# Optimization experiments

Measured on AMD Instinct MI355X. Metric: run time of the kernel, lower is better.

The kernel has to match this reference:

```python
import jax, jax.numpy as jnp
import numpy as np

N = 50000   # nodes
E = 800000  # edges (avg degree 16)
H = 128     # hidden


def setup_inputs() -> dict:
    key = jax.random.key(0)
    k1, k2, k3, k4, k5 = jax.random.split(key, 5)
    s = 1.0 / np.sqrt(H).astype(np.float32)
    x = jax.random.normal(k1, (N, H), dtype=jnp.float32)
    edge_index = jax.random.randint(k2, (2, E), 0, N, dtype=jnp.int64)
    a_i = jax.random.normal(k3, (H,), dtype=jnp.float32) * s
    a_j = jax.random.normal(k4, (H,), dtype=jnp.float32) * s
    W = jax.random.normal(k5, (H, H), dtype=jnp.float32) * s
    return {"x": x, "edge_index": edge_index, "a_i": a_i, "a_j": a_j, "W": W}


def reference(x, edge_index, a_i, a_j, W):
    n = x.shape[0]
    idx_j = edge_index[0]  # row of sparse adj (output node)
    idx_i = edge_index[1]  # col of sparse adj (source node, softmax segment)

    # per-node attention scores, gathered per edge
    si = x @ a_i  # [N]
    sj = x @ a_j  # [N]
    e = jax.nn.leaky_relu(si[idx_i] + sj[idx_j], negative_slope=0.01)  # [E]

    # segment softmax over idx_i (numerically stable)
    seg_max = jax.ops.segment_max(e, idx_i, num_segments=n)
    e_exp = jnp.exp(e - seg_max[idx_i])
    denom = jax.ops.segment_sum(e_exp, idx_i, num_segments=n)
    alpha = e_exp / denom[idx_i]  # [E]

    # messages and sparse aggregation: out[j] += alpha * m[i]
    m = x + x @ W  # [N, H]
    out = jax.ops.segment_sum(alpha[:, None] * m[idx_i], idx_j, num_segments=n)

    # exact (erf) GELU to match torch nn.GELU default; dropout is identity in eval
    return jax.nn.gelu(out, approximate=False)
```

## Files before the change

kernel.cpp:

```cpp
#include <hip/hip_runtime.h>
#include <hip/hip_fp16.h>
#include <math.h>

#define HDIM 128
#define NB   32
#define CAP  768
#define BINB 256
#define DG   64
#define WIN  12544

typedef __attribute__((ext_vector_type(8))) short short8;
typedef __attribute__((ext_vector_type(4))) float f32x4;

__device__ __forceinline__ float gelu_f(float v) {
    return 0.5f * v * (1.0f + erff(v * 0.70710678118654752440f));
}
__device__ __forceinline__ unsigned bf_rne(float f) {
    unsigned u = __float_as_uint(f);
    return (u + 0x7fffu + ((u >> 16) & 1u)) >> 16;
}
__device__ __forceinline__ float bf_lo(unsigned u) {
    return __uint_as_float(u << 16);
}
__device__ __forceinline__ float bf_hi(unsigned u) {
    return __uint_as_float(u & 0xffff0000u);
}

__global__ void __launch_bounds__(256) k_scores(
    const float* __restrict__ x, const float* __restrict__ a_i,
    const float* __restrict__ a_j, float* __restrict__ si,
    float* __restrict__ sj, unsigned* __restrict__ xbp,
    unsigned* __restrict__ gcnt, int N) {
    if (blockIdx.x == 0)
        for (int w = threadIdx.x; w < 2048; w += 256) gcnt[w] = 0u;
    const int wave = threadIdx.x >> 6;
    const int lane = threadIdx.x & 63;
    const int n = blockIdx.x * 4 + wave;
    if (n >= N) return;
    const float xa = x[(size_t)n * HDIM + lane];
    const float xb = x[(size_t)n * HDIM + 64 + lane];
    xbp[(size_t)n * 64 + lane] = bf_rne(xa) | (bf_rne(xb) << 16);
    float vi = xa * a_i[lane] + xb * a_i[64 + lane];
    float vj = xa * a_j[lane] + xb * a_j[64 + lane];
    #pragma unroll
    for (int d = 32; d; d >>= 1) {
        vi += __shfl_xor(vi, d, 64);
        vj += __shfl_xor(vj, d, 64);
    }
    if (lane == 0) {
        si[n] = vi;
        sj[n] = vj;
    }
}

__global__ void __launch_bounds__(1024) k_bin(
    const int* __restrict__ idx_i, const int* __restrict__ idx_j,
    const float* __restrict__ si, const float* __restrict__ sj,
    unsigned short* __restrict__ exbuf, unsigned* __restrict__ gcnt,
    uint2* __restrict__ edges, int nbuk, int E_) {
    __shared__ unsigned cnt_l[2048];
    const int blk = blockIdx.x;
    const int chunk = (E_ + BINB - 1) / BINB;
    const int e0 = blk * chunk;
    const int e1 = min(e0 + chunk, E_);
    for (int w = threadIdx.x; w < nbuk; w += 1024) cnt_l[w] = 0u;
    __syncthreads();
    uint2 rec[4];
    int   bl[4];
    #pragma unroll
    for (int k = 0; k < 4; ++k) {
        const int t = e0 + threadIdx.x + k * 1024;
        bl[k] = -1;
        if (t < e1) {
            const int i = idx_i[t];
            const int j = idx_j[t];
            float e = si[i] + sj[j];
            e = (e > 0.f) ? e : 0.01f * e;
            const float ex = __expf(e);
            exbuf[t] = __half_as_ushort(__float2half(ex));
            const int b = j >> 5;
            atomicAdd(&cnt_l[b], 1u);
            rec[k] = make_uint2((unsigned)i | ((unsigned)(j & 31) << 24),
                                __float_as_uint(ex));
            bl[k] = b;
        }
    }
    for (int t = e0 + threadIdx.x + 4 * 1024; t < e1; t += 1024) {
        const int i = idx_i[t];
        const int j = idx_j[t];
        float e = si[i] + sj[j];
        e = (e > 0.f) ? e : 0.01f * e;
        const float ex = __expf(e);
        exbuf[t] = __half_as_ushort(__float2half(ex));
        const int b = j >> 5;
        const unsigned slot = min(atomicAdd(&gcnt[b], 1u), (unsigned)(CAP - 1));
        edges[(size_t)b * CAP + slot] = make_uint2(
            (unsigned)i | ((unsigned)(j & 31) << 24), __float_as_uint(ex));
    }
    __syncthreads();
    for (int w = threadIdx.x; w < nbuk; w += 1024) {
        const unsigned c = cnt_l[w];
        cnt_l[w] = c ? atomicAdd(&gcnt[w], c) : 0u;
    }
    __syncthreads();
    #pragma unroll
    for (int k = 0; k < 4; ++k) {
        if (bl[k] >= 0) {
            const unsigned slot =
                min(atomicAdd(&cnt_l[bl[k]], 1u), (unsigned)(CAP - 1));
            edges[(size_t)bl[k] * CAP + slot] = rec[k];
        }
    }
}

__global__ void __launch_bounds__(1024) k_den(
    const int* __restrict__ idx_i, const unsigned short* __restrict__ exbuf,
    float* __restrict__ denp, int N, int E_) {
    __shared__ float dl[WIN];
    const int b = blockIdx.x;
    const int chunk = (E_ + DG - 1) / DG;
    const int e0 = b * chunk;
    const int e1 = min(e0 + chunk, E_);
    for (int pass = 0; pass < 4; ++pass) {
        const int lo = pass * WIN;
        for (int w = threadIdx.x; w < WIN; w += 1024) dl[w] = 0.f;
        __syncthreads();
        for (int t = e0 + threadIdx.x; t < e1; t += 1024) {
            const int i = idx_i[t];
            const unsigned rel = (unsigned)(i - lo);
            if (rel < (unsigned)WIN)
                atomicAdd(&dl[rel], __half2float(__ushort_as_half(exbuf[t])));
        }
        __syncthreads();
        for (int w = threadIdx.x; w < WIN && lo + w < N; w += 1024)
            denp[(size_t)b * N + lo + w] = dl[w];
        __syncthreads();
    }
}

__global__ void __launch_bounds__(256) k_denred(const float* __restrict__ denp,
                                                float* __restrict__ denom,
                                                int N) {
    const int v = blockIdx.x * 256 + threadIdx.x;
    if (v >= N) return;
    float s = 0.f;
    for (int b = 0; b < DG; ++b) s += denp[(size_t)b * N + v];
    denom[v] = s;
}

__global__ void __launch_bounds__(256) k_gemm(
    const unsigned* __restrict__ xbp, const float* __restrict__ Wm,
    const float* __restrict__ denom, unsigned* __restrict__ mbp, int N) {
    __shared__ unsigned wl[128][68];
    const int t = threadIdx.x;
    {
        const int n = t & 127;
        const int h = t >> 7;
        for (int w = h * 32; w < h * 32 + 32; ++w) {
            const float f0 = Wm[w * 128 + n];
            const float f1 = Wm[(w + 64) * 128 + n];
            wl[n][w] = bf_rne(f0) | (bf_rne(f1) << 16);
        }
    }
    __syncthreads();
    const int wave = t >> 6;
    const int lane = t & 63;
    const int q = lane >> 4;
    const int m16 = lane & 15;
    const int r0 = blockIdx.x * 64 + wave * 16;
    if (r0 >= N) return;
    const int rowA = min(r0 + m16, N - 1);
    union { uint4 u; short8 s; } a[4];
    #pragma unroll
    for (int kb = 0; kb < 4; ++kb)
        a[kb].u = *(const uint4*)(xbp + (size_t)rowA * 64 + kb * 16 + q * 4);
    f32x4 acc[8];
    #pragma unroll
    for (int c = 0; c < 8; ++c) acc[c] = (f32x4){0.f, 0.f, 0.f, 0.f};
    #pragma unroll
    for (int kb = 0; kb < 4; ++kb) {
        #pragma unroll
        for (int c = 0; c < 8; ++c) {
            const short8 bfr =
                *(const short8*)&wl[c * 16 + m16][kb * 16 + q * 4];
            acc[c] = __builtin_amdgcn_mfma_f32_16x16x32_bf16(
                a[kb].s, bfr, acc[c], 0, 0, 0);
        }
    }
    #pragma unroll
    for (int r = 0; r < 4; ++r) {
        const int row = r0 + q * 4 + r;
        if (row >= N) continue;
        const float rdv = 1.0f / denom[row];
        #pragma unroll
        for (int c = 0; c < 4; ++c) {
            const int w = m16 + 16 * c;
            const unsigned xv = xbp[(size_t)row * 64 + w];
            const float vlo = (bf_lo(xv) + acc[c][r]) * rdv;
            const float vhi = (bf_hi(xv) + acc[c + 4][r]) * rdv;
            mbp[(size_t)row * 64 + w] = bf_rne(vlo) | (bf_rne(vhi) << 16);
        }
    }
}

__global__ void __launch_bounds__(512) k_agg(
    const unsigned* __restrict__ gcnt, const uint2* __restrict__ edges,
    const unsigned* __restrict__ mbp, float* __restrict__ out, int N) {
    __shared__ uint2 srec[CAP];
    __shared__ unsigned cnt_l[NB];
    __shared__ unsigned off_l[NB];
    const int b = blockIdx.x;
    const int cntb = min((int)gcnt[b], CAP);
    const uint2* eb = edges + (size_t)b * CAP;
    if (threadIdx.x < NB) cnt_l[threadIdx.x] = 0u;
    __syncthreads();
    uint2 r0_ = make_uint2(0u, 0u), r1_ = make_uint2(0u, 0u);
    int jl0 = -1, jl1 = -1, kl0 = 0, kl1 = 0;
    {
        const int t0 = threadIdx.x;
        if (t0 < cntb) {
            r0_ = eb[t0];
            jl0 = (int)(r0_.x >> 24);
            kl0 = (int)atomicAdd(&cnt_l[jl0], 1u);
        }
        const int t1 = threadIdx.x + 512;
        if (t1 < cntb) {
            r1_ = eb[t1];
            jl1 = (int)(r1_.x >> 24);
            kl1 = (int)atomicAdd(&cnt_l[jl1], 1u);
        }
    }
    __syncthreads();
    if (threadIdx.x < NB) {
        const unsigned v = cnt_l[threadIdx.x];
        unsigned s = v;
        #pragma unroll
        for (int d = 1; d < NB; d <<= 1) {
            const unsigned o = __shfl_up(s, d, 64);
            if ((int)threadIdx.x >= d) s += o;
        }
        off_l[threadIdx.x] = s - v;
    }
    __syncthreads();
    if (jl0 >= 0) srec[off_l[jl0] + kl0] = r0_;
    if (jl1 >= 0) srec[off_l[jl1] + kl1] = r1_;
    __syncthreads();
    const int wave = threadIdx.x >> 6;
    const int lane = threadIdx.x & 63;
    for (int nr = wave; nr < NB; nr += 8) {
        const int n = (b << 5) + nr;
        if (n >= N) continue;
        const int p0 = (int)off_l[nr];
        const int p1 = p0 + (int)cnt_l[nr];
        float ax = 0.f, ay = 0.f;
        int p = p0;
        for (; p + 8 <= p1; p += 8) {
            const uint2 e0 = srec[p];
            const uint2 e1 = srec[p + 1];
            const uint2 e2 = srec[p + 2];
            const uint2 e3 = srec[p + 3];
            const uint2 e4 = srec[p + 4];
            const uint2 e5 = srec[p + 5];
            const uint2 e6 = srec[p + 6];
            const uint2 e7 = srec[p + 7];
            const unsigned u0 = mbp[(size_t)(e0.x & 0xffffffu) * 64 + lane];
            const unsigned u1 = mbp[(size_t)(e1.x & 0xffffffu) * 64 + lane];
            const unsigned u2 = mbp[(size_t)(e2.x & 0xffffffu) * 64 + lane];
            const unsigned u3 = mbp[(size_t)(e3.x & 0xffffffu) * 64 + lane];
            const unsigned u4 = mbp[(size_t)(e4.x & 0xffffffu) * 64 + lane];
            const unsigned u5 = mbp[(size_t)(e5.x & 0xffffffu) * 64 + lane];
            const unsigned u6 = mbp[(size_t)(e6.x & 0xffffffu) * 64 + lane];
            const unsigned u7 = mbp[(size_t)(e7.x & 0xffffffu) * 64 + lane];
            ax = fmaf(__uint_as_float(e0.y), bf_lo(u0), ax);
            ay = fmaf(__uint_as_float(e0.y), bf_hi(u0), ay);
            ax = fmaf(__uint_as_float(e1.y), bf_lo(u1), ax);
            ay = fmaf(__uint_as_float(e1.y), bf_hi(u1), ay);
            ax = fmaf(__uint_as_float(e2.y), bf_lo(u2), ax);
            ay = fmaf(__uint_as_float(e2.y), bf_hi(u2), ay);
            ax = fmaf(__uint_as_float(e3.y), bf_lo(u3), ax);
            ay = fmaf(__uint_as_float(e3.y), bf_hi(u3), ay);
            ax = fmaf(__uint_as_float(e4.y), bf_lo(u4), ax);
            ay = fmaf(__uint_as_float(e4.y), bf_hi(u4), ay);
            ax = fmaf(__uint_as_float(e5.y), bf_lo(u5), ax);
            ay = fmaf(__uint_as_float(e5.y), bf_hi(u5), ay);
            ax = fmaf(__uint_as_float(e6.y), bf_lo(u6), ax);
            ay = fmaf(__uint_as_float(e6.y), bf_hi(u6), ay);
            ax = fmaf(__uint_as_float(e7.y), bf_lo(u7), ax);
            ay = fmaf(__uint_as_float(e7.y), bf_hi(u7), ay);
        }
        for (; p + 4 <= p1; p += 4) {
            const uint2 e0 = srec[p];
            const uint2 e1 = srec[p + 1];
            const uint2 e2 = srec[p + 2];
            const uint2 e3 = srec[p + 3];
            const unsigned u0 = mbp[(size_t)(e0.x & 0xffffffu) * 64 + lane];
            const unsigned u1 = mbp[(size_t)(e1.x & 0xffffffu) * 64 + lane];
            const unsigned u2 = mbp[(size_t)(e2.x & 0xffffffu) * 64 + lane];
            const unsigned u3 = mbp[(size_t)(e3.x & 0xffffffu) * 64 + lane];
            ax = fmaf(__uint_as_float(e0.y), bf_lo(u0), ax);
            ay = fmaf(__uint_as_float(e0.y), bf_hi(u0), ay);
            ax = fmaf(__uint_as_float(e1.y), bf_lo(u1), ax);
            ay = fmaf(__uint_as_float(e1.y), bf_hi(u1), ay);
            ax = fmaf(__uint_as_float(e2.y), bf_lo(u2), ax);
            ay = fmaf(__uint_as_float(e2.y), bf_hi(u2), ay);
            ax = fmaf(__uint_as_float(e3.y), bf_lo(u3), ax);
            ay = fmaf(__uint_as_float(e3.y), bf_hi(u3), ay);
        }
        for (; p < p1; ++p) {
            const uint2 e = srec[p];
            const unsigned u = mbp[(size_t)(e.x & 0xffffffu) * 64 + lane];
            const float a = __uint_as_float(e.y);
            ax = fmaf(a, bf_lo(u), ax);
            ay = fmaf(a, bf_hi(u), ay);
        }
        out[(size_t)n * HDIM + lane] = gelu_f(ax);
        out[(size_t)n * HDIM + 64 + lane] = gelu_f(ay);
    }
}

extern "C" void kernel_launch(void* const* d_in, const int* in_sizes, int n_in,
                              void* d_out, int out_size, void* d_ws,
                              size_t ws_size, hipStream_t stream) {
    const float* x   = (const float*)d_in[0];
    const int*   eix = (const int*)d_in[1];
    const float* a_i = (const float*)d_in[2];
    const float* a_j = (const float*)d_in[3];
    const float* Wm  = (const float*)d_in[4];
    float* out = (float*)d_out;

    const int N = in_sizes[0] / HDIM;
    const int E = in_sizes[1] / 2;
    const int nbuk = (N + NB - 1) / NB;

    unsigned* xbp  = (unsigned*)d_ws;
    unsigned* mbp  = xbp + (size_t)N * 64;
    float* denp    = (float*)(mbp + (size_t)N * 64);
    float* si      = denp + (size_t)DG * N;
    float* sj      = si + N;
    float* denom   = sj + N;
    unsigned* gcnt = (unsigned*)(denom + N);
    unsigned short* exbuf = (unsigned short*)(gcnt + 2048);
    uint2* edges   = (uint2*)(exbuf + ((E + 7) & ~7));

    const int* idx_j = eix;
    const int* idx_i = eix + E;

    k_scores<<<(N + 3) / 4, 256, 0, stream>>>(x, a_i, a_j, si, sj, xbp, gcnt,
                                              N);
    k_bin<<<BINB, 1024, 0, stream>>>(idx_i, idx_j, si, sj, exbuf, gcnt, edges,
                                     nbuk, E);
    k_den<<<DG, 1024, 0, stream>>>(idx_i, exbuf, denp, N, E);
    k_denred<<<(N + 255) / 256, 256, 0, stream>>>(denp, denom, N);
    k_gemm<<<(N + 63) / 64, 256, 0, stream>>>(xbp, Wm, denom, mbp, N);
    k_agg<<<nbuk, 512, 0, stream>>>(gcnt, edges, mbp, out, N);
}
```

Baseline: 180.7 us.

## Replace atomic edge binning with count-scan-scatter and split denominator passes across blocks

Edge bucketing now runs in three kernels: per-block bucket counts, a per-bucket prefix scan over blocks, then a scatter that takes slots from shared-memory cursors seeded by the scan. This removes global atomics on bucket counters and gives deterministic per-block placement. It costs two extra launches, a second read of the edge indices and exbuf, and ex is stored as a half-rounded value. Separately, the denominator kernel's four sequential window passes become four independent block groups, giving 256 blocks instead of 64 for more parallelism.

```diff
diff --git a/kernel.cpp b/kernel.cpp
--- a/kernel.cpp
+++ b/kernel.cpp
@@ -29,10 +29,7 @@
 __global__ void __launch_bounds__(256) k_scores(
     const float* __restrict__ x, const float* __restrict__ a_i,
     const float* __restrict__ a_j, float* __restrict__ si,
-    float* __restrict__ sj, unsigned* __restrict__ xbp,
-    unsigned* __restrict__ gcnt, int N) {
-    if (blockIdx.x == 0)
-        for (int w = threadIdx.x; w < 2048; w += 256) gcnt[w] = 0u;
+    float* __restrict__ sj, unsigned* __restrict__ xbp, int N) {
     const int wave = threadIdx.x >> 6;
     const int lane = threadIdx.x & 63;
     const int n = blockIdx.x * 4 + wave;
@@ -53,11 +50,11 @@
     }
 }
 
-__global__ void __launch_bounds__(1024) k_bin(
+__global__ void __launch_bounds__(1024) k_binA(
     const int* __restrict__ idx_i, const int* __restrict__ idx_j,
     const float* __restrict__ si, const float* __restrict__ sj,
-    unsigned short* __restrict__ exbuf, unsigned* __restrict__ gcnt,
-    uint2* __restrict__ edges, int nbuk, int E_) {
+    unsigned short* __restrict__ exbuf, unsigned* __restrict__ cnt_g,
+    int nbuk, int E_) {
     __shared__ unsigned cnt_l[2048];
     const int blk = blockIdx.x;
     const int chunk = (E_ + BINB - 1) / BINB;
@@ -65,51 +62,66 @@
     const int e1 = min(e0 + chunk, E_);
     for (int w = threadIdx.x; w < nbuk; w += 1024) cnt_l[w] = 0u;
     __syncthreads();
-    uint2 rec[4];
-    int   bl[4];
-    #pragma unroll
-    for (int k = 0; k < 4; ++k) {
-        const int t = e0 + threadIdx.x + k * 1024;
-        bl[k] = -1;
-        if (t < e1) {
-            const int i = idx_i[t];
-            const int j = idx_j[t];
-            float e = si[i] + sj[j];
-            e = (e > 0.f) ? e : 0.01f * e;
-            const float ex = __expf(e);
-            exbuf[t] = __half_as_ushort(__float2half(ex));
-            const int b = j >> 5;
-            atomicAdd(&cnt_l[b], 1u);
-            rec[k] = make_uint2((unsigned)i | ((unsigned)(j & 31) << 24),
-                                __float_as_uint(ex));
-            bl[k] = b;
-        }
-    }
-    for (int t = e0 + threadIdx.x + 4 * 1024; t < e1; t += 1024) {
+    for (int t = e0 + threadIdx.x; t < e1; t += 1024) {
         const int i = idx_i[t];
         const int j = idx_j[t];
         float e = si[i] + sj[j];
         e = (e > 0.f) ? e : 0.01f * e;
         const float ex = __expf(e);
         exbuf[t] = __half_as_ushort(__float2half(ex));
+        atomicAdd(&cnt_l[j >> 5], 1u);
+    }
+    __syncthreads();
+    for (int w = threadIdx.x; w < nbuk; w += 1024)
+        cnt_g[(size_t)blk * nbuk + w] = cnt_l[w];
+}
+
+__global__ void __launch_bounds__(256) k_scan(
+    const unsigned* __restrict__ cnt_g, unsigned* __restrict__ base_t,
+    unsigned* __restrict__ gcnt, int nbuk) {
+    const int bucket = blockIdx.x;
+    const int t = threadIdx.x;
+    const int lane = t & 63;
+    const int wave = t >> 6;
+    const unsigned v = cnt_g[(size_t)t * nbuk + bucket];
+    unsigned s = v;
+    #pragma unroll
+    for (int d = 1; d < 64; d <<= 1) {
+        const unsigned o = __shfl_up(s, d, 64);
+        if (lane >= d) s += o;
+    }
+    __shared__ unsigned wsum[4];
+    if (lane == 63) wsum[wave] = s;
+    __syncthreads();
+    unsigned add = 0;
+    #pragma unroll
+    for (int w = 0; w < 4; ++w)
+        if (w < wave) add += wsum[w];
+    base_t[(size_t)t * nbuk + bucket] = add + s - v;
+    if (t == 255) gcnt[bucket] = add + s;
+}
+
+__global__ void __launch_bounds__(1024) k_binB(
+    const int* __restrict__ idx_i, const int* __restrict__ idx_j,
+    const unsigned short* __restrict__ exbuf,
+    const unsigned* __restrict__ base_t, uint2* __restrict__ edges,
+    int nbuk, int E_) {
+    __shared__ unsigned cur[2048];
+    const int blk = blockIdx.x;
+    const int chunk = (E_ + BINB - 1) / BINB;
+    const int e0 = blk * chunk;
+    const int e1 = min(e0 + chunk, E_);
+    for (int w = threadIdx.x; w < nbuk; w += 1024)
+        cur[w] = base_t[(size_t)blk * nbuk + w];
+    __syncthreads();
+    for (int t = e0 + threadIdx.x; t < e1; t += 1024) {
+        const int i = idx_i[t];
+        const int j = idx_j[t];
+        const float ex = __half2float(__ushort_as_half(exbuf[t]));
         const int b = j >> 5;
-        const unsigned slot = min(atomicAdd(&gcnt[b], 1u), (unsigned)(CAP - 1));
+        const unsigned slot = min(atomicAdd(&cur[b], 1u), (unsigned)(CAP - 1));
         edges[(size_t)b * CAP + slot] = make_uint2(
             (unsigned)i | ((unsigned)(j & 31) << 24), __float_as_uint(ex));
-    }
-    __syncthreads();
-    for (int w = threadIdx.x; w < nbuk; w += 1024) {
-        const unsigned c = cnt_l[w];
-        cnt_l[w] = c ? atomicAdd(&gcnt[w], c) : 0u;
-    }
-    __syncthreads();
-    #pragma unroll
-    for (int k = 0; k < 4; ++k) {
-        if (bl[k] >= 0) {
-            const unsigned slot =
-                min(atomicAdd(&cnt_l[bl[k]], 1u), (unsigned)(CAP - 1));
-            edges[(size_t)bl[k] * CAP + slot] = rec[k];
-        }
     }
 }
 
@@ -117,25 +129,21 @@
     const int* __restrict__ idx_i, const unsigned short* __restrict__ exbuf,
     float* __restrict__ denp, int N, int E_) {
     __shared__ float dl[WIN];
-    const int b = blockIdx.x;
+    const int cid = blockIdx.x & (DG - 1);
+    const int lo = (blockIdx.x >> 6) * WIN;
     const int chunk = (E_ + DG - 1) / DG;
-    const int e0 = b * chunk;
+    const int e0 = cid * chunk;
     const int e1 = min(e0 + chunk, E_);
-    for (int pass = 0; pass < 4; ++pass) {
-        const int lo = pass * WIN;
-        for (int w = threadIdx.x; w < WIN; w += 1024) dl[w] = 0.f;
-        __syncthreads();
-        for (int t = e0 + threadIdx.x; t < e1; t += 1024) {
-            const int i = idx_i[t];
-            const unsigned rel = (unsigned)(i - lo);
-            if (rel < (unsigned)WIN)
-                atomicAdd(&dl[rel], __half2float(__ushort_as_half(exbuf[t])));
-        }
-        __syncthreads();
-        for (int w = threadIdx.x; w < WIN && lo + w < N; w += 1024)
-            denp[(size_t)b * N + lo + w] = dl[w];
-        __syncthreads();
-    }
+    for (int w = threadIdx.x; w < WIN; w += 1024) dl[w] = 0.f;
+    __syncthreads();
+    for (int t = e0 + threadIdx.x; t < e1; t += 1024) {
+        const unsigned rel = (unsigned)(idx_i[t] - lo);
+        if (rel < (unsigned)WIN)
+            atomicAdd(&dl[rel], __half2float(__ushort_as_half(exbuf[t])));
+    }
+    __syncthreads();
+    for (int w = threadIdx.x; w < WIN && lo + w < N; w += 1024)
+        denp[(size_t)cid * N + lo + w] = dl[w];
 }
 
 __global__ void __launch_bounds__(256) k_denred(const float* __restrict__ denp,
@@ -332,24 +340,29 @@
     const int E = in_sizes[1] / 2;
     const int nbuk = (N + NB - 1) / NB;
 
-    unsigned* xbp  = (unsigned*)d_ws;
-    unsigned* mbp  = xbp + (size_t)N * 64;
-    float* denp    = (float*)(mbp + (size_t)N * 64);
-    float* si      = denp + (size_t)DG * N;
-    float* sj      = si + N;
-    float* denom   = sj + N;
-    unsigned* gcnt = (unsigned*)(denom + N);
-    unsigned short* exbuf = (unsigned short*)(gcnt + 2048);
-    uint2* edges   = (uint2*)(exbuf + ((E + 7) & ~7));
+    unsigned* xbp   = (unsigned*)d_ws;
+    unsigned* mbp   = xbp + (size_t)N * 64;
+    float* denp     = (float*)(mbp + (size_t)N * 64);
+    float* si       = denp + (size_t)DG * N;
+    float* sj       = si + N;
+    float* denom    = sj + N;
+    unsigned* cnt_g = (unsigned*)(denom + N);
+    unsigned* base_t = cnt_g + (size_t)BINB * nbuk;
+    unsigned* gcnt  = base_t + (size_t)BINB * nbuk;
+    unsigned short* exbuf =
+        (unsigned short*)(gcnt + ((nbuk + 7) & ~7));
+    uint2* edges    = (uint2*)(exbuf + ((E + 7) & ~7));
 
     const int* idx_j = eix;
     const int* idx_i = eix + E;
 
-    k_scores<<<(N + 3) / 4, 256, 0, stream>>>(x, a_i, a_j, si, sj, xbp, gcnt,
-                                              N);
-    k_bin<<<BINB, 1024, 0, stream>>>(idx_i, idx_j, si, sj, exbuf, gcnt, edges,
-                                     nbuk, E);
-    k_den<<<DG, 1024, 0, stream>>>(idx_i, exbuf, denp, N, E);
+    k_scores<<<(N + 3) / 4, 256, 0, stream>>>(x, a_i, a_j, si, sj, xbp, N);
+    k_binA<<<BINB, 1024, 0, stream>>>(idx_i, idx_j, si, sj, exbuf, cnt_g,
+                                      nbuk, E);
+    k_scan<<<nbuk, 256, 0, stream>>>(cnt_g, base_t, gcnt, nbuk);
+    k_binB<<<BINB, 1024, 0, stream>>>(idx_i, idx_j, exbuf, base_t, edges,
+                                      nbuk, E);
+    k_den<<<DG * 4, 1024, 0, stream>>>(idx_i, exbuf, denp, N, E);
     k_denred<<<(N + 255) / 256, 256, 0, stream>>>(denp, denom, N);
     k_gemm<<<(N + 63) / 64, 256, 0, stream>>>(xbp, Wm, denom, mbp, N);
     k_agg<<<nbuk, 512, 0, stream>>>(gcnt, edges, mbp, out, N);
```

Measured after the change: 169.6 us. 1.07x faster.
